# Performance work log

Hardware: AMD Instinct MI355X
Metric: run time of the kernel (lower is better)

Reference implementation:

```python
import jax, jax.numpy as jnp
import numpy as np

CH = 256
B, H, W = 8, 64, 64


def _conv1x1(x, w, b):
    # x: [b, cin, h, w], w: [cout, cin], b: [cout]
    return jnp.einsum('bchw,oc->bohw', x, w) + b[None, :, None, None]


def setup_inputs() -> dict:
    key = jax.random.key(0)
    ks = jax.random.split(key, 6)
    s = 0.05  # weight scale (spectral-norm keeps weights O(1); scaled for stable softmax)
    return {
        'x': jax.random.normal(ks[0], (B, CH, H, W), dtype=jnp.float32),
        'wf': jax.random.normal(ks[1], (CH // 8, CH), dtype=jnp.float32) * s,
        'bf': jnp.zeros((CH // 8,), dtype=jnp.float32),
        'wg': jax.random.normal(ks[2], (CH // 8, CH), dtype=jnp.float32) * s,
        'bg': jnp.zeros((CH // 8,), dtype=jnp.float32),
        'wh': jax.random.normal(ks[3], (CH // 2, CH), dtype=jnp.float32) * s,
        'bh': jnp.zeros((CH // 2,), dtype=jnp.float32),
        'wv': jax.random.normal(ks[4], (CH, CH // 2), dtype=jnp.float32) * s,
        'bv': jnp.zeros((CH,), dtype=jnp.float32),
        'gamma': jnp.ones((1,), dtype=jnp.float32) * 0.5,
    }


def reference(x, wf, bf, wg, bg, wh, bh, wv, bv, gamma):
    b, c, h, w = x.shape
    n = h * w
    f = _conv1x1(x, wf, bf).reshape(b, -1, n)   # [b, c/8, n]
    g = _conv1x1(x, wg, bg).reshape(b, -1, n)   # [b, c/8, n]
    # scores = f^T g : [b, n, n]; softmax over last dim
    beta = jax.nn.softmax(jnp.einsum('bkn,bkm->bnm', f, g), axis=-1)
    h_ = _conv1x1(x, wh, bh).reshape(b, -1, n)  # [b, c/2, n]
    o = jnp.einsum('bcn,bnm->bcm', h_, beta).reshape(b, c // 2, h, w)
    o = _conv1x1(o, wv, bv)                      # [b, c, h, w]
    return x + gamma[0] * o
```

## Files before the change

kernel.cpp:

```cpp
#include <hip/hip_runtime.h>
#include <cstdint>

typedef float f32x4 __attribute__((ext_vector_type(4)));
typedef short bf16x8 __attribute__((ext_vector_type(8)));
typedef unsigned short u16x4 __attribute__((ext_vector_type(4)));
typedef unsigned uint4v __attribute__((ext_vector_type(4)));
typedef unsigned uint2v __attribute__((ext_vector_type(2)));

#define LOG2E 1.44269504088896340736f

#if __has_builtin(__builtin_amdgcn_exp2f)
#define EXP2(v) __builtin_amdgcn_exp2f(v)
#else
#define EXP2(v) exp2f(v)
#endif
#if __has_builtin(__builtin_amdgcn_logf)
#define LOG2F(v) __builtin_amdgcn_logf(v)
#else
#define LOG2F(v) __log2f(v)
#endif

#define GLD16(gp, lp) __builtin_amdgcn_global_load_lds( \
    (const __attribute__((address_space(1))) unsigned*)(const void*)(gp), \
    (__attribute__((address_space(3))) unsigned*)(void*)(lp), 16, 0, 0)

enum : unsigned {
    WALL_OFF  = 0u,
    BALL_OFF  = 98304u,
    WVF_OFF   = 99072u,
    FF_OFF    = 164608u,
    GF_OFF    = 2261760u,
    HF_OFF    = 4358912u,
    ZPART_OFF = 12878592u,
    PART_OFF  = 13404928u,
};

static __device__ __forceinline__ unsigned short f2bf(float f) {
    unsigned u = __builtin_bit_cast(unsigned, f);
    u += 0x7fffu + ((u >> 16) & 1u);
    return (unsigned short)(u >> 16);
}

static __device__ __forceinline__ unsigned pk_bf(float lo, float hi) {
    unsigned a = __builtin_bit_cast(unsigned, hi) + 0x8000u;
    unsigned b = __builtin_bit_cast(unsigned, lo) + 0x8000u;
    return __builtin_amdgcn_perm(a, b, 0x07060302u);
}

static __device__ __forceinline__ f32x4 mfma_bf16(bf16x8 a, bf16x8 b, f32x4 c) {
    return __builtin_amdgcn_mfma_f32_16x16x32_bf16(a, b, c, 0, 0, 0);
}

__global__ __launch_bounds__(256) void k0_pack(const float* __restrict__ wf,
                                               const float* __restrict__ bfv,
                                               const float* __restrict__ wg,
                                               const float* __restrict__ bg,
                                               const float* __restrict__ wh,
                                               const float* __restrict__ bh,
                                               const float* __restrict__ wv,
                                               unsigned char* __restrict__ ws) {
    unsigned idx = blockIdx.x * 256u + threadIdx.x;
    unsigned short* Wall = (unsigned short*)(ws + WALL_OFF);
    float* ball = (float*)(ws + BALL_OFF);
    unsigned short* wvf = (unsigned short*)(ws + WVF_OFF);
    if (idx < 49152u) {
        unsigned k = idx >> 8;
        float v;
        if (k < 32u)      v = wf[idx] * LOG2E;
        else if (k < 64u) v = wg[idx - 8192u];
        else              v = wh[idx - 16384u];
        Wall[idx] = f2bf(v);
    } else if (idx < 49344u) {
        unsigned k = idx - 49152u;
        float v;
        if (k < 32u)      v = bfv[k] * LOG2E;
        else if (k < 64u) v = bg[k - 32u];
        else              v = bh[k - 64u];
        ball[k] = v;
    } else if (idx < 82112u) {
        unsigned jj = idx - 49344u;
        unsigned cc = jj >> 7, c = jj & 127u;
        unsigned cct = cc >> 4, lv = cc & 15u;
        unsigned ksv = c >> 5, qv = (c >> 3) & 3u, jv = c & 7u;
        wvf[(((cct * 4u + ksv) * 4u + qv) * 16u + lv) * 8u + jv] = f2bf(wv[jj]);
    }
}

__global__ __launch_bounds__(256) void k1_proj(const float* __restrict__ x,
                                               unsigned char* __restrict__ ws) {
    __shared__ unsigned XT[64 * 132];
    const int b = blockIdx.y;
    const int n0 = blockIdx.x * 64;
    const unsigned short* Wall = (const unsigned short*)(ws + WALL_OFF);
    const float* ball = (const float*)(ws + BALL_OFF);
    unsigned short* Ff = (unsigned short*)(ws + FF_OFF) + b * 131072;
    unsigned short* Gf = (unsigned short*)(ws + GF_OFF) + b * 131072;
    unsigned short* Hf = (unsigned short*)(ws + HF_OFF) + b * 524288;
    const int tid = threadIdx.x;
    const float* xb = x + b * (256 * 4096) + n0;
    {
        const int n4 = (tid & 15) * 4;
        const int crow = (tid >> 4) * 2;
        #pragma unroll
        for (int it = 0; it < 8; ++it) {
            const int c = crow + it * 32;
            const f32x4 r0 = *(const f32x4*)&xb[(size_t)c * 4096 + n4];
            const f32x4 r1 = *(const f32x4*)&xb[(size_t)(c + 1) * 4096 + n4];
            #pragma unroll
            for (int j = 0; j < 4; ++j)
                XT[(n4 + j) * 132 + (c >> 1)] = pk_bf(r0[j], r1[j]);
        }
    }
    __syncthreads();
    const int l = tid & 15, q = (tid >> 4) & 3, w = tid >> 6;
    const int nloc = w * 16 + l;
    const int ncol = n0 + nloc;
    bf16x8 bX[8];
    #pragma unroll
    for (int ks = 0; ks < 8; ++ks)
        bX[ks] = *(const bf16x8*)&XT[nloc * 132 + ks * 16 + q * 4];
    #pragma unroll
    for (int kt = 0; kt < 12; ++kt) {
        f32x4 acc = {0.f, 0.f, 0.f, 0.f};
        #pragma unroll
        for (int ks = 0; ks < 8; ++ks) {
            bf16x8 aW = *(const bf16x8*)&Wall[(kt * 16 + l) * 256 + ks * 32 + q * 8];
            acc = mfma_bf16(aW, bX[ks], acc);
        }
        const int kr0 = kt * 16 + q * 4;
        #pragma unroll
        for (int r = 0; r < 4; ++r) acc[r] += ball[kr0 + r];
        if (kt < 4) {
            const int kk = kt & 1;
            unsigned short* dst = (kt < 2) ? Ff : Gf;
            const int nt = ncol >> 4;
            const int qf = kk * 2 + (q >> 1), j0 = (q & 1) * 4;
            u16x4 pk;
            #pragma unroll
            for (int r = 0; r < 4; ++r) pk[r] = f2bf(acc[r]);
            *(u16x4*)&dst[(nt * 64 + qf * 16 + l) * 8 + j0] = pk;
        } else {
            const int ct = kt - 4;
            const int nt = ncol >> 5, qh = (ncol >> 3) & 3, jh = ncol & 7;
            #pragma unroll
            for (int r = 0; r < 4; ++r)
                Hf[((nt * 8 + ct) * 64 + qh * 16 + (q * 4 + r)) * 8 + jh] = f2bf(acc[r]);
        }
    }
}

__global__ __launch_bounds__(256) void k2_stats(unsigned char* __restrict__ ws) {
    const int b = blockIdx.y, zsl = blockIdx.z, tid = threadIdx.x;
    const int lane = tid & 63, l = tid & 15, q = (tid >> 4) & 3, w = tid >> 6;
    const unsigned short* Ff = (const unsigned short*)(ws + FF_OFF) + b * 131072;
    const unsigned short* Gf = (const unsigned short*)(ws + GF_OFF) + b * 131072;
    float* Zp = (float*)(ws + ZPART_OFF) + zsl * 32768 + b * 4096;
    const int n0 = blockIdx.x * 256 + w * 64;
    const int nt0 = n0 >> 4;
    bf16x8 aF[4];
    #pragma unroll
    for (int t = 0; t < 4; ++t)
        aF[t] = *(const bf16x8*)&Ff[((nt0 + t) * 64 + lane) * 8];
    f32x4 z[4];
    #pragma unroll
    for (int t = 0; t < 4; ++t) z[t] = (f32x4){0.f, 0.f, 0.f, 0.f};
    const int mt0 = zsl * 64;
    bf16x8 bG = *(const bf16x8*)&Gf[(mt0 * 64 + lane) * 8];
    for (int mt = 0; mt < 64; ++mt) {
        const bf16x8 g = bG;
        if (mt + 1 < 64)
            bG = *(const bf16x8*)&Gf[((mt0 + mt + 1) * 64 + lane) * 8];
        #pragma unroll
        for (int t = 0; t < 4; ++t) {
            f32x4 s = mfma_bf16(aF[t], g, (f32x4){0.f, 0.f, 0.f, 0.f});
            #pragma unroll
            for (int r = 0; r < 4; ++r)
                z[t][r] += EXP2(s[r]);
        }
    }
    #pragma unroll
    for (int off = 1; off < 16; off <<= 1)
        #pragma unroll
        for (int t = 0; t < 4; ++t)
            #pragma unroll
            for (int r = 0; r < 4; ++r)
                z[t][r] += __shfl_xor(z[t][r], off, 64);
    if (l == 0) {
        #pragma unroll
        for (int t = 0; t < 4; ++t)
            #pragma unroll
            for (int r = 0; r < 4; ++r)
                Zp[n0 + t * 16 + q * 4 + r] = z[t][r];
    }
}

template<int NS>
__global__ __launch_bounds__(256, 4) void k3_attn(unsigned char* __restrict__ ws) {
    constexpr int NITER = 128 / NS;
    constexpr int NGRP = 8 * NS;
    constexpr int NQ = 4096 / NS;
    __shared__ __align__(16) unsigned short HT[2][4096];
    __shared__ __align__(16) unsigned short FTs[2][1024];
    __shared__ __align__(16) float SC[NQ];
    const int tid = threadIdx.x;
    const int lane = tid & 63, l = tid & 15, q = (tid >> 4) & 3, w = tid >> 6;
    const int g = blockIdx.x % NGRP, bxm = blockIdx.x / NGRP;
    const int b = g / NS, nh = g % NS;
    const unsigned short* Ff = (const unsigned short*)(ws + FF_OFF) + b * 131072;
    const unsigned short* Gf = (const unsigned short*)(ws + GF_OFF) + b * 131072;
    const unsigned short* Hf = (const unsigned short*)(ws + HF_OFF) + b * 524288;
    const int mt0 = bxm * 8 + w * 2;
    const bf16x8 bG0 = *(const bf16x8*)&Gf[(mt0 * 64 + lane) * 8];
    const bf16x8 bG1 = *(const bf16x8*)&Gf[((mt0 + 1) * 64 + lane) * 8];
    f32x4 acc0[8], acc1[8];
    #pragma unroll
    for (int ct = 0; ct < 8; ++ct) {
        acc0[ct] = (f32x4){0.f, 0.f, 0.f, 0.f};
        acc1[ct] = (f32x4){0.f, 0.f, 0.f, 0.f};
    }
    const bool qlo = q < 2;
    const int srcA = (q & 1) * 32 + l;
    const int srcB = srcA + 16;

    auto stage = [&](int i, int p) {
        const unsigned short* Hg = Hf + (size_t)(nh * NITER + i) * 4096;
        GLD16(Hg + ((w * 2 + 0) * 64 + lane) * 8, &HT[p][(w * 2 + 0) * 512]);
        GLD16(Hg + ((w * 2 + 1) * 64 + lane) * 8, &HT[p][(w * 2 + 1) * 512]);
        if (w < 2)
            GLD16(Ff + ((size_t)((nh * NITER + i) * 2 + w) * 64 + lane) * 8,
                  &FTs[p][w * 512]);
    };

    stage(0, 0);
    {
        const float* zp = (const float*)(ws + ZPART_OFF) + b * 4096 + nh * NQ;
        #pragma unroll
        for (int j = tid; j < NQ; j += 256) {
            const float s = zp[j] + zp[32768 + j] + zp[65536 + j] + zp[98304 + j];
            SC[j] = -LOG2F(s);
        }
    }

    for (int i = 0; i < NITER; ++i) {
        const int p = i & 1;
        __syncthreads();
        if (i + 1 < NITER) stage(i + 1, p ^ 1);
        const bf16x8 aF0 = *(const bf16x8*)&FTs[p][lane * 8];
        const bf16x8 aF1 = *(const bf16x8*)&FTs[p][512 + lane * 8];
        const f32x4 c0 = *(const f32x4*)&SC[i * 32 + q * 4];
        const f32x4 c1 = *(const f32x4*)&SC[i * 32 + 16 + q * 4];
        f32x4 s0 = mfma_bf16(aF0, bG0, c0);
        f32x4 s1 = mfma_bf16(aF1, bG0, c1);
        f32x4 s2 = mfma_bf16(aF0, bG1, c0);
        f32x4 s3 = mfma_bf16(aF1, bG1, c1);
        f32x4 e0, e1, e2, e3;
        #pragma unroll
        for (int r = 0; r < 4; ++r) {
            e0[r] = EXP2(s0[r]);
            e1[r] = EXP2(s1[r]);
            e2[r] = EXP2(s2[r]);
            e3[r] = EXP2(s3[r]);
        }
        const unsigned a01 = pk_bf(e0[0], e0[1]), a23 = pk_bf(e0[2], e0[3]);
        const unsigned b01 = pk_bf(e1[0], e1[1]), b23 = pk_bf(e1[2], e1[3]);
        const unsigned g01 = pk_bf(e2[0], e2[1]), g23 = pk_bf(e2[2], e2[3]);
        const unsigned h01 = pk_bf(e3[0], e3[1]), h23 = pk_bf(e3[2], e3[3]);
        uint4v r0, r1;
        {
            int tA, tB;
            tA = __shfl((int)a01, srcA, 64); tB = __shfl((int)b01, srcA, 64);
            r0[0] = (unsigned)(qlo ? tA : tB);
            tA = __shfl((int)a23, srcA, 64); tB = __shfl((int)b23, srcA, 64);
            r0[1] = (unsigned)(qlo ? tA : tB);
            tA = __shfl((int)a01, srcB, 64); tB = __shfl((int)b01, srcB, 64);
            r0[2] = (unsigned)(qlo ? tA : tB);
            tA = __shfl((int)a23, srcB, 64); tB = __shfl((int)b23, srcB, 64);
            r0[3] = (unsigned)(qlo ? tA : tB);
            tA = __shfl((int)g01, srcA, 64); tB = __shfl((int)h01, srcA, 64);
            r1[0] = (unsigned)(qlo ? tA : tB);
            tA = __shfl((int)g23, srcA, 64); tB = __shfl((int)h23, srcA, 64);
            r1[1] = (unsigned)(qlo ? tA : tB);
            tA = __shfl((int)g01, srcB, 64); tB = __shfl((int)h01, srcB, 64);
            r1[2] = (unsigned)(qlo ? tA : tB);
            tA = __shfl((int)g23, srcB, 64); tB = __shfl((int)h23, srcB, 64);
            r1[3] = (unsigned)(qlo ? tA : tB);
        }
        const bf16x8 bE0 = __builtin_bit_cast(bf16x8, r0);
        const bf16x8 bE1 = __builtin_bit_cast(bf16x8, r1);
        #pragma unroll
        for (int ct = 0; ct < 8; ++ct) {
            const bf16x8 aH = *(const bf16x8*)&HT[p][ct * 512 + lane * 8];
            acc0[ct] = mfma_bf16(aH, bE0, acc0[ct]);
            acc1[ct] = mfma_bf16(aH, bE1, acc1[ct]);
        }
    }
    unsigned short* P = (unsigned short*)(ws + PART_OFF);
    const size_t mb = (size_t)(b * NS + nh) * 4096 + bxm * 128;
    #pragma unroll
    for (int ct = 0; ct < 8; ++ct) {
        uint2v p0, p1;
        p0[0] = pk_bf(acc0[ct][0], acc0[ct][1]);
        p0[1] = pk_bf(acc0[ct][2], acc0[ct][3]);
        p1[0] = pk_bf(acc1[ct][0], acc1[ct][1]);
        p1[1] = pk_bf(acc1[ct][2], acc1[ct][3]);
        *(uint2v*)&P[(mb + w * 32 + l) * 128 + ct * 16 + q * 4] = p0;
        *(uint2v*)&P[(mb + w * 32 + 16 + l) * 128 + ct * 16 + q * 4] = p1;
    }
}

template<int NS>
__global__ __launch_bounds__(256) void k4_out(const float* __restrict__ x,
                                              const float* __restrict__ bv,
                                              const float* __restrict__ gamma,
                                              float* __restrict__ out,
                                              unsigned char* __restrict__ ws) {
    const int b = blockIdx.y, tid = threadIdx.x;
    const int lane = tid & 63, l = tid & 15, q = (tid >> 4) & 3, w = tid >> 6;
    const unsigned short* P = (const unsigned short*)(ws + PART_OFF);
    const unsigned short* Wvf = (const unsigned short*)(ws + WVF_OFF);
    const int mg = blockIdx.x * 64 + w * 16 + l;
    bf16x8 bO[4];
    #pragma unroll
    for (int ks = 0; ks < 4; ++ks) {
        float lo[4] = {0.f, 0.f, 0.f, 0.f}, hi[4] = {0.f, 0.f, 0.f, 0.f};
        #pragma unroll
        for (int h = 0; h < NS; ++h) {
            const size_t bh = ((size_t)(b * NS + h) * 4096 + mg) * 128;
            const uint4v u = *(const uint4v*)&P[bh + ks * 32 + q * 8];
            #pragma unroll
            for (int j = 0; j < 4; ++j) {
                lo[j] += __builtin_bit_cast(float, u[j] << 16);
                hi[j] += __builtin_bit_cast(float, u[j] & 0xffff0000u);
            }
        }
        uint4v s;
        #pragma unroll
        for (int j = 0; j < 4; ++j) s[j] = pk_bf(lo[j], hi[j]);
        bO[ks] = __builtin_bit_cast(bf16x8, s);
    }
    const float gam = gamma[0];
    const float* xb = x + b * (256 * 4096);
    float* ob = out + b * (256 * 4096);
    #pragma unroll
    for (int cct = 0; cct < 16; ++cct) {
        f32x4 f = {0.f, 0.f, 0.f, 0.f};
        #pragma unroll
        for (int ks = 0; ks < 4; ++ks) {
            const bf16x8 aV = *(const bf16x8*)&Wvf[((cct * 4 + ks) * 64 + lane) * 8];
            f = mfma_bf16(aV, bO[ks], f);
        }
        #pragma unroll
        for (int r = 0; r < 4; ++r) {
            const int cc = cct * 16 + q * 4 + r;
            ob[cc * 4096 + mg] = xb[cc * 4096 + mg] + gam * (f[r] + bv[cc]);
        }
    }
}

extern "C" void kernel_launch(void* const* d_in, const int* in_sizes, int n_in,
                              void* d_out, int out_size, void* d_ws, size_t ws_size,
                              hipStream_t stream) {
    const float* x   = (const float*)d_in[0];
    const float* wf  = (const float*)d_in[1];
    const float* bfv = (const float*)d_in[2];
    const float* wg  = (const float*)d_in[3];
    const float* bg  = (const float*)d_in[4];
    const float* wh  = (const float*)d_in[5];
    const float* bh  = (const float*)d_in[6];
    const float* wv  = (const float*)d_in[7];
    const float* bv  = (const float*)d_in[8];
    const float* gam = (const float*)d_in[9];
    float* out = (float*)d_out;
    unsigned char* ws = (unsigned char*)d_ws;
    (void)in_sizes; (void)n_in; (void)out_size;

    hipLaunchKernelGGL(k0_pack, dim3(321), dim3(256), 0, stream,
                       wf, bfv, wg, bg, wh, bh, wv, ws);
    hipLaunchKernelGGL(k1_proj, dim3(64, 8), dim3(256), 0, stream, x, ws);
    hipLaunchKernelGGL(k2_stats, dim3(16, 8, 4), dim3(256), 0, stream, ws);

    const size_t base = (size_t)PART_OFF;
    const size_t per  = (size_t)8 * 4096 * 128 * 2;
    if (ws_size >= base + 8 * per) {
        hipLaunchKernelGGL(HIP_KERNEL_NAME(k3_attn<8>), dim3(2048), dim3(256),
                           0, stream, ws);
        hipLaunchKernelGGL(HIP_KERNEL_NAME(k4_out<8>), dim3(64, 8), dim3(256),
                           0, stream, x, bv, gam, out, ws);
    } else if (ws_size >= base + 4 * per) {
        hipLaunchKernelGGL(HIP_KERNEL_NAME(k3_attn<4>), dim3(1024), dim3(256),
                           0, stream, ws);
        hipLaunchKernelGGL(HIP_KERNEL_NAME(k4_out<4>), dim3(64, 8), dim3(256),
                           0, stream, x, bv, gam, out, ws);
    } else {
        hipLaunchKernelGGL(HIP_KERNEL_NAME(k3_attn<2>), dim3(512), dim3(256),
                           0, stream, ws);
        hipLaunchKernelGGL(HIP_KERNEL_NAME(k4_out<2>), dim3(64, 8), dim3(256),
                           0, stream, x, bv, gam, out, ws);
    }
}
```

Baseline: 247.9 us.

## Use 16x16x16 bf16 MFMA in attention to drop cross-lane shuffles; cap split at 4

After: 211.0 us. 1.18x faster.

```diff
diff --git a/kernel.cpp b/kernel.cpp
--- a/kernel.cpp
+++ b/kernel.cpp
@@ -3,6 +3,7 @@
 
 typedef float f32x4 __attribute__((ext_vector_type(4)));
 typedef short bf16x8 __attribute__((ext_vector_type(8)));
+typedef short bf16x4 __attribute__((ext_vector_type(4)));
 typedef unsigned short u16x4 __attribute__((ext_vector_type(4)));
 typedef unsigned uint4v __attribute__((ext_vector_type(4)));
 typedef unsigned uint2v __attribute__((ext_vector_type(2)));
@@ -18,6 +19,15 @@
 #define LOG2F(v) __builtin_amdgcn_logf(v)
 #else
 #define LOG2F(v) __log2f(v)
+#endif
+
+#if __has_builtin(__builtin_amdgcn_mfma_f32_16x16x16bf16_1k)
+#define HK16 1
+static __device__ __forceinline__ f32x4 mfma16(bf16x4 a, bf16x4 b, f32x4 c) {
+    return __builtin_amdgcn_mfma_f32_16x16x16bf16_1k(a, b, c, 0, 0, 0);
+}
+#else
+#define HK16 0
 #endif
 
 #define GLD16(gp, lp) __builtin_amdgcn_global_load_lds( \
@@ -141,10 +151,19 @@
             *(u16x4*)&dst[(nt * 64 + qf * 16 + l) * 8 + j0] = pk;
         } else {
             const int ct = kt - 4;
-            const int nt = ncol >> 5, qh = (ncol >> 3) & 3, jh = ncol & 7;
+            const int nt = ncol >> 5;
+#if HK16
+            const int qn = (ncol >> 2) & 3, jn = ncol & 3, half = (ncol >> 4) & 1;
+            #pragma unroll
+            for (int r = 0; r < 4; ++r)
+                Hf[((nt * 8 + ct) * 64 + qn * 16 + (q * 4 + r)) * 8 + half * 4 + jn]
+                    = f2bf(acc[r]);
+#else
+            const int qh = (ncol >> 3) & 3, jh = ncol & 7;
             #pragma unroll
             for (int r = 0; r < 4; ++r)
                 Hf[((nt * 8 + ct) * 64 + qh * 16 + (q * 4 + r)) * 8 + jh] = f2bf(acc[r]);
+#endif
         }
     }
 }
@@ -218,9 +237,11 @@
         acc0[ct] = (f32x4){0.f, 0.f, 0.f, 0.f};
         acc1[ct] = (f32x4){0.f, 0.f, 0.f, 0.f};
     }
+#if !HK16
     const bool qlo = q < 2;
     const int srcA = (q & 1) * 32 + l;
     const int srcB = srcA + 16;
+#endif
 
     auto stage = [&](int i, int p) {
         const unsigned short* Hg = Hf + (size_t)(nh * NITER + i) * 4096;
@@ -261,6 +282,26 @@
             e2[r] = EXP2(s2[r]);
             e3[r] = EXP2(s3[r]);
         }
+#if HK16
+        uint2v u00 = {pk_bf(e0[0], e0[1]), pk_bf(e0[2], e0[3])};
+        uint2v u01 = {pk_bf(e1[0], e1[1]), pk_bf(e1[2], e1[3])};
+        uint2v u10 = {pk_bf(e2[0], e2[1]), pk_bf(e2[2], e2[3])};
+        uint2v u11 = {pk_bf(e3[0], e3[1]), pk_bf(e3[2], e3[3])};
+        const bf16x4 B00 = __builtin_bit_cast(bf16x4, u00);
+        const bf16x4 B01 = __builtin_bit_cast(bf16x4, u01);
+        const bf16x4 B10 = __builtin_bit_cast(bf16x4, u10);
+        const bf16x4 B11 = __builtin_bit_cast(bf16x4, u11);
+        #pragma unroll
+        for (int ct = 0; ct < 8; ++ct) {
+            const bf16x8 hv = *(const bf16x8*)&HT[p][ct * 512 + lane * 8];
+            const bf16x4 h0 = __builtin_shufflevector(hv, hv, 0, 1, 2, 3);
+            const bf16x4 h1 = __builtin_shufflevector(hv, hv, 4, 5, 6, 7);
+            acc0[ct] = mfma16(h0, B00, acc0[ct]);
+            acc0[ct] = mfma16(h1, B01, acc0[ct]);
+            acc1[ct] = mfma16(h0, B10, acc1[ct]);
+            acc1[ct] = mfma16(h1, B11, acc1[ct]);
+        }
+#else
         const unsigned a01 = pk_bf(e0[0], e0[1]), a23 = pk_bf(e0[2], e0[3]);
         const unsigned b01 = pk_bf(e1[0], e1[1]), b23 = pk_bf(e1[2], e1[3]);
         const unsigned g01 = pk_bf(e2[0], e2[1]), g23 = pk_bf(e2[2], e2[3]);
@@ -293,6 +334,7 @@
             acc0[ct] = mfma_bf16(aH, bE0, acc0[ct]);
             acc1[ct] = mfma_bf16(aH, bE1, acc1[ct]);
         }
+#endif
     }
     unsigned short* P = (unsigned short*)(ws + PART_OFF);
     const size_t mb = (size_t)(b * NS + nh) * 4096 + bxm * 128;
@@ -381,12 +423,7 @@
 
     const size_t base = (size_t)PART_OFF;
     const size_t per  = (size_t)8 * 4096 * 128 * 2;
-    if (ws_size >= base + 8 * per) {
-        hipLaunchKernelGGL(HIP_KERNEL_NAME(k3_attn<8>), dim3(2048), dim3(256),
-                           0, stream, ws);
-        hipLaunchKernelGGL(HIP_KERNEL_NAME(k4_out<8>), dim3(64, 8), dim3(256),
-                           0, stream, x, bv, gam, out, ws);
-    } else if (ws_size >= base + 4 * per) {
+    if (ws_size >= base + 4 * per) {
         hipLaunchKernelGGL(HIP_KERNEL_NAME(k3_attn<4>), dim3(1024), dim3(256),
                            0, stream, ws);
         hipLaunchKernelGGL(HIP_KERNEL_NAME(k4_out<4>), dim3(64, 8), dim3(256),
```
